# Optimization experiments

Hardware: AMD Instinct MI355X
Metric: run time of the kernel (lower is better)

The kernel has to match this reference:

```python
import jax, jax.numpy as jnp
import numpy as np

ALPHA = 0.001  # heb_lr
EPS = 1e-12    # F.normalize default eps


def setup_inputs() -> dict:
    key = jax.random.key(0)
    k1, k2 = jax.random.split(key)
    x = jax.random.normal(k1, (1, 8192), dtype=jnp.float32)
    # fc.weight ~ Uniform(0, 0.5), shape [out_dim, in_dim]
    W = jax.random.uniform(k2, (4096, 8192), dtype=jnp.float32) * 0.5
    return {"x": x, "W": W}


def reference(x, W):
    # Linear projection (no bias): [1, in] @ [in, out] -> [1, out]
    y = x @ W.T
    # F.normalize(y, p=2, dim=1)
    nrm = jnp.maximum(jnp.linalg.norm(y, axis=1, keepdims=True), EPS)
    y_n = y / nrm

    # Hebbian / Sanger (GHA) weight update, using the INITIAL weight for the
    # decorrelation term (as in the torch code).
    yv = y_n[0]  # [out]
    xv = x[0]    # [in]
    # einsum('jk,lkm,m->jl', W^T, itensors, y) with itensors[l,k,m]=1 iff k==m<=l
    # is exactly a cumulative sum over k of W[k, :] * y[k]  -> [out, in]
    sanger = yv[:, None] * jnp.cumsum(W * yv[:, None], axis=0)
    W_new = W + ALPHA * (jnp.outer(yv, xv) - sanger)
    return y_n, W_new
```

## Files before the change

kernel.cpp:

```cpp
#include <hip/hip_runtime.h>
#include <math.h>

#define ALPHA 0.001f
#define EPS 1e-12f
#define IN_DIM 8192
#define OUT_DIM 4096
#define COL4 (IN_DIM / 4)
#define NSEG 128
#define SEG_ROWS (OUT_DIM / NSEG)

typedef float f32x4 __attribute__((ext_vector_type(4)));

__global__ __launch_bounds__(256) void k_matvec(const float* __restrict__ W,
                                                const float* __restrict__ x,
                                                float* __restrict__ y) {
    const int wave = threadIdx.x >> 6;
    const int lane = threadIdx.x & 63;
    const int row = blockIdx.x * 4 + wave;
    const float4* Wr = (const float4*)(W + (size_t)row * IN_DIM);
    const float4* xv = (const float4*)x;
    float acc = 0.0f;
#pragma unroll 8
    for (int c = 0; c < COL4 / 64; ++c) {
        float4 w = Wr[lane + c * 64];
        float4 xx = xv[lane + c * 64];
        acc += w.x * xx.x + w.y * xx.y + w.z * xx.z + w.w * xx.w;
    }
#pragma unroll
    for (int off = 32; off; off >>= 1) acc += __shfl_xor(acc, off, 64);
    if (lane == 0) y[row] = acc;
}

__global__ __launch_bounds__(256) void k_norm(const float* __restrict__ y,
                                              float* __restrict__ yn_out,
                                              float* __restrict__ yv_ws) {
    __shared__ float red[4];
    float s = 0.0f;
    for (int i = threadIdx.x; i < OUT_DIM; i += 256) {
        float v = y[i];
        s += v * v;
    }
#pragma unroll
    for (int off = 32; off; off >>= 1) s += __shfl_xor(s, off, 64);
    const int wave = threadIdx.x >> 6;
    const int lane = threadIdx.x & 63;
    if (lane == 0) red[wave] = s;
    __syncthreads();
    const float tot = red[0] + red[1] + red[2] + red[3];
    const float inv = 1.0f / fmaxf(sqrtf(tot), EPS);
    for (int i = threadIdx.x; i < OUT_DIM; i += 256) {
        float v = y[i] * inv;
        yn_out[i] = v;
        yv_ws[i] = v;
    }
}

__global__ __launch_bounds__(256) void k_pseg(const float* __restrict__ W,
                                              const float* __restrict__ yv,
                                              float* __restrict__ P) {
    const int seg = blockIdx.y;
    const int col4 = blockIdx.x * 256 + threadIdx.x;
    const float4* Wp = (const float4*)W;
    const int j0 = seg * SEG_ROWS;
    float4 acc = make_float4(0.f, 0.f, 0.f, 0.f);
#pragma unroll 4
    for (int j = 0; j < SEG_ROWS; ++j) {
        const float yj = yv[j0 + j];
        float4 w = Wp[(size_t)(j0 + j) * COL4 + col4];
        acc.x += w.x * yj;
        acc.y += w.y * yj;
        acc.z += w.z * yj;
        acc.w += w.w * yj;
    }
    ((float4*)P)[(size_t)seg * COL4 + col4] = acc;
}

__global__ __launch_bounds__(64) void k_scan(float* __restrict__ P) {
    const int col4 = blockIdx.x * 64 + threadIdx.x;
    float4* Pp = (float4*)P;
    float4 run = make_float4(0.f, 0.f, 0.f, 0.f);
#pragma unroll 8
    for (int s = 0; s < NSEG; ++s) {
        float4 v = Pp[(size_t)s * COL4 + col4];
        Pp[(size_t)s * COL4 + col4] = run;
        run.x += v.x;
        run.y += v.y;
        run.z += v.z;
        run.w += v.w;
    }
}

__global__ __launch_bounds__(512) void k_update(const float* __restrict__ W,
                                                const float* __restrict__ x,
                                                const float* __restrict__ yv,
                                                const float* __restrict__ E,
                                                float* __restrict__ Wout) {
    const int seg = blockIdx.y;
    const int col4 = blockIdx.x * 512 + threadIdx.x;
    const float4* Wp = (const float4*)W;
    f32x4* Op = (f32x4*)Wout;
    float4 run = ((const float4*)E)[(size_t)seg * COL4 + col4];
    const float4 x4 = ((const float4*)x)[col4];
    const int j0 = seg * SEG_ROWS;
#pragma unroll 4
    for (int j = 0; j < SEG_ROWS; ++j) {
        const float yj = yv[j0 + j];
        const float aj = ALPHA * yj;
        const size_t idx = (size_t)(j0 + j) * COL4 + col4;
        float4 w = Wp[idx];
        run.x += w.x * yj;
        run.y += w.y * yj;
        run.z += w.z * yj;
        run.w += w.w * yj;
        f32x4 o;
        o.x = w.x + aj * (x4.x - run.x);
        o.y = w.y + aj * (x4.y - run.y);
        o.z = w.z + aj * (x4.z - run.z);
        o.w = w.w + aj * (x4.w - run.w);
        __builtin_nontemporal_store(o, &Op[idx]);
    }
}

extern "C" void kernel_launch(void* const* d_in, const int* in_sizes, int n_in,
                              void* d_out, int out_size, void* d_ws, size_t ws_size,
                              hipStream_t stream) {
    const float* x = (const float*)d_in[0];
    const float* W = (const float*)d_in[1];
    float* out = (float*)d_out;
    float* yn_out = out;
    float* Wout = out + OUT_DIM;

    float* y = (float*)d_ws;
    float* P = y + OUT_DIM;

    k_matvec<<<dim3(OUT_DIM / 4), dim3(256), 0, stream>>>(W, x, y);
    k_norm<<<dim3(1), dim3(256), 0, stream>>>(y, yn_out, y);
    k_pseg<<<dim3(COL4 / 256, NSEG), dim3(256), 0, stream>>>(W, y, P);
    k_scan<<<dim3(32), dim3(64), 0, stream>>>(P);
    k_update<<<dim3(COL4 / 512, NSEG), dim3(512), 0, stream>>>(W, x, y, P, Wout);
}
```

Measured before the change: 284.5 us.

## Fuse matvec with segment partial sums and defer normalization into update

The matvec and the per-segment weighted column sums now run in one kernel. Each block owns 8 full rows, computes the unnormalized y for each row, and reuses the same W loads to accumulate the partial prefix sums, so W is read twice instead of three times. The normalization is folded algebraically into the update kernel: the scale factors inv and inv² are applied there, and the norm kernel is replaced by a sum-of-squares pass inside the scan kernel. The partial buffer grows to 512 segments, which makes the serial scan longer and adds per-row block barriers in the fused kernel.

```diff
diff --git a/kernel.cpp b/kernel.cpp
--- a/kernel.cpp
+++ b/kernel.cpp
@@ -6,118 +6,132 @@
 #define IN_DIM 8192
 #define OUT_DIM 4096
 #define COL4 (IN_DIM / 4)
-#define NSEG 128
-#define SEG_ROWS (OUT_DIM / NSEG)
+#define NSEG 512
+#define SEG_ROWS 8
 
 typedef float f32x4 __attribute__((ext_vector_type(4)));
 
-__global__ __launch_bounds__(256) void k_matvec(const float* __restrict__ W,
-                                                const float* __restrict__ x,
-                                                float* __restrict__ y) {
-    const int wave = threadIdx.x >> 6;
-    const int lane = threadIdx.x & 63;
-    const int row = blockIdx.x * 4 + wave;
-    const float4* Wr = (const float4*)(W + (size_t)row * IN_DIM);
-    const float4* xv = (const float4*)x;
-    float acc = 0.0f;
-#pragma unroll 8
-    for (int c = 0; c < COL4 / 64; ++c) {
-        float4 w = Wr[lane + c * 64];
-        float4 xx = xv[lane + c * 64];
-        acc += w.x * xx.x + w.y * xx.y + w.z * xx.z + w.w * xx.w;
+#define WS_Y   0
+#define WS_SSQ (OUT_DIM)
+#define WS_P   (OUT_DIM + 16)
+
+__global__ __launch_bounds__(512, 4) void kA(const float* __restrict__ W,
+                                             const float* __restrict__ x,
+                                             float* __restrict__ y,
+                                             float* __restrict__ P) {
+    const int s = blockIdx.x;
+    const int t = threadIdx.x;
+    const int wv = t >> 6, ln = t & 63;
+    __shared__ float red[2][8];
+
+    const float4* W4 = (const float4*)W;
+    const float4* X4 = (const float4*)x;
+
+    float4 xr[4];
+#pragma unroll
+    for (int c = 0; c < 4; ++c) xr[c] = X4[c * 512 + t];
+
+    float4 acc[4];
+#pragma unroll
+    for (int c = 0; c < 4; ++c) acc[c] = make_float4(0.f, 0.f, 0.f, 0.f);
+
+    const int j0 = s * SEG_ROWS;
+#pragma unroll
+    for (int j = 0; j < SEG_ROWS; ++j) {
+        float4 w[4];
+#pragma unroll
+        for (int c = 0; c < 4; ++c)
+            w[c] = W4[(size_t)(j0 + j) * COL4 + c * 512 + t];
+        float p = 0.f;
+#pragma unroll
+        for (int c = 0; c < 4; ++c)
+            p += w[c].x * xr[c].x + w[c].y * xr[c].y +
+                 w[c].z * xr[c].z + w[c].w * xr[c].w;
+#pragma unroll
+        for (int off = 32; off; off >>= 1) p += __shfl_xor(p, off, 64);
+        if (ln == 0) red[j & 1][wv] = p;
+        __syncthreads();
+        float yj = 0.f;
+#pragma unroll
+        for (int k = 0; k < 8; ++k) yj += red[j & 1][k];
+        if (t == 0) y[j0 + j] = yj;
+#pragma unroll
+        for (int c = 0; c < 4; ++c) {
+            acc[c].x += w[c].x * yj;
+            acc[c].y += w[c].y * yj;
+            acc[c].z += w[c].z * yj;
+            acc[c].w += w[c].w * yj;
+        }
     }
+    float4* P4 = (float4*)P;
 #pragma unroll
-    for (int off = 32; off; off >>= 1) acc += __shfl_xor(acc, off, 64);
-    if (lane == 0) y[row] = acc;
+    for (int c = 0; c < 4; ++c)
+        P4[(size_t)s * COL4 + c * 512 + t] = acc[c];
 }
 
-__global__ __launch_bounds__(256) void k_norm(const float* __restrict__ y,
-                                              float* __restrict__ yn_out,
-                                              float* __restrict__ yv_ws) {
-    __shared__ float red[4];
-    float s = 0.0f;
-    for (int i = threadIdx.x; i < OUT_DIM; i += 256) {
-        float v = y[i];
-        s += v * v;
+__global__ __launch_bounds__(64) void kB(float* __restrict__ P,
+                                         const float* __restrict__ y,
+                                         float* __restrict__ ssq) {
+    if (blockIdx.x == 0) {
+        float q = 0.f;
+        for (int i = threadIdx.x; i < OUT_DIM; i += 64) {
+            const float v = y[i];
+            q += v * v;
+        }
+#pragma unroll
+        for (int off = 32; off; off >>= 1) q += __shfl_xor(q, off, 64);
+        if (threadIdx.x == 0) *ssq = q;
     }
-#pragma unroll
-    for (int off = 32; off; off >>= 1) s += __shfl_xor(s, off, 64);
-    const int wave = threadIdx.x >> 6;
-    const int lane = threadIdx.x & 63;
-    if (lane == 0) red[wave] = s;
-    __syncthreads();
-    const float tot = red[0] + red[1] + red[2] + red[3];
-    const float inv = 1.0f / fmaxf(sqrtf(tot), EPS);
-    for (int i = threadIdx.x; i < OUT_DIM; i += 256) {
-        float v = y[i] * inv;
-        yn_out[i] = v;
-        yv_ws[i] = v;
+    const int c4 = blockIdx.x * 64 + threadIdx.x;
+    float4* P4 = (float4*)P;
+    float4 run = make_float4(0.f, 0.f, 0.f, 0.f);
+#pragma unroll 8
+    for (int s = 0; s < NSEG; ++s) {
+        const float4 v = P4[(size_t)s * COL4 + c4];
+        P4[(size_t)s * COL4 + c4] = run;
+        run.x += v.x; run.y += v.y; run.z += v.z; run.w += v.w;
     }
 }
 
-__global__ __launch_bounds__(256) void k_pseg(const float* __restrict__ W,
-                                              const float* __restrict__ yv,
-                                              float* __restrict__ P) {
-    const int seg = blockIdx.y;
-    const int col4 = blockIdx.x * 256 + threadIdx.x;
-    const float4* Wp = (const float4*)W;
-    const int j0 = seg * SEG_ROWS;
-    float4 acc = make_float4(0.f, 0.f, 0.f, 0.f);
-#pragma unroll 4
+__global__ __launch_bounds__(512, 4) void kC(const float* __restrict__ W,
+                                             const float* __restrict__ x,
+                                             const float* __restrict__ y,
+                                             const float* __restrict__ P,
+                                             const float* __restrict__ ssq,
+                                             float* __restrict__ yn,
+                                             float* __restrict__ Wout) {
+    const int s = blockIdx.y;
+    const int t = threadIdx.x;
+    const int c4 = blockIdx.x * 512 + t;
+    const float inv = 1.f / fmaxf(sqrtf(*ssq), EPS);
+    const float a_s = ALPHA * inv;
+    const float b_s = ALPHA * inv * inv;
+    const int j0 = s * SEG_ROWS;
+
+    if (blockIdx.x == 0 && t < SEG_ROWS) {
+        yn[j0 + t] = y[j0 + t] * inv;
+    }
+
+    const float4* W4 = (const float4*)W;
+    const float4* X4 = (const float4*)x;
+    f32x4* O4 = (f32x4*)Wout;
+    float4 run = ((const float4*)P)[(size_t)s * COL4 + c4];
+    const float4 x4 = X4[c4];
+#pragma unroll
     for (int j = 0; j < SEG_ROWS; ++j) {
-        const float yj = yv[j0 + j];
-        float4 w = Wp[(size_t)(j0 + j) * COL4 + col4];
-        acc.x += w.x * yj;
-        acc.y += w.y * yj;
-        acc.z += w.z * yj;
-        acc.w += w.w * yj;
-    }
-    ((float4*)P)[(size_t)seg * COL4 + col4] = acc;
-}
-
-__global__ __launch_bounds__(64) void k_scan(float* __restrict__ P) {
-    const int col4 = blockIdx.x * 64 + threadIdx.x;
-    float4* Pp = (float4*)P;
-    float4 run = make_float4(0.f, 0.f, 0.f, 0.f);
-#pragma unroll 8
-    for (int s = 0; s < NSEG; ++s) {
-        float4 v = Pp[(size_t)s * COL4 + col4];
-        Pp[(size_t)s * COL4 + col4] = run;
-        run.x += v.x;
-        run.y += v.y;
-        run.z += v.z;
-        run.w += v.w;
-    }
-}
-
-__global__ __launch_bounds__(512) void k_update(const float* __restrict__ W,
-                                                const float* __restrict__ x,
-                                                const float* __restrict__ yv,
-                                                const float* __restrict__ E,
-                                                float* __restrict__ Wout) {
-    const int seg = blockIdx.y;
-    const int col4 = blockIdx.x * 512 + threadIdx.x;
-    const float4* Wp = (const float4*)W;
-    f32x4* Op = (f32x4*)Wout;
-    float4 run = ((const float4*)E)[(size_t)seg * COL4 + col4];
-    const float4 x4 = ((const float4*)x)[col4];
-    const int j0 = seg * SEG_ROWS;
-#pragma unroll 4
-    for (int j = 0; j < SEG_ROWS; ++j) {
-        const float yj = yv[j0 + j];
-        const float aj = ALPHA * yj;
-        const size_t idx = (size_t)(j0 + j) * COL4 + col4;
-        float4 w = Wp[idx];
-        run.x += w.x * yj;
-        run.y += w.y * yj;
-        run.z += w.z * yj;
-        run.w += w.w * yj;
+        const float yj = y[j0 + j];
+        const float aj = a_s * yj;
+        const float bj = b_s * yj;
+        const size_t idx = (size_t)(j0 + j) * COL4 + c4;
+        const float4 w = W4[idx];
+        run.x += w.x * yj; run.y += w.y * yj;
+        run.z += w.z * yj; run.w += w.w * yj;
         f32x4 o;
-        o.x = w.x + aj * (x4.x - run.x);
-        o.y = w.y + aj * (x4.y - run.y);
-        o.z = w.z + aj * (x4.z - run.z);
-        o.w = w.w + aj * (x4.w - run.w);
-        __builtin_nontemporal_store(o, &Op[idx]);
+        o.x = w.x + aj * x4.x - bj * run.x;
+        o.y = w.y + aj * x4.y - bj * run.y;
+        o.z = w.z + aj * x4.z - bj * run.z;
+        o.w = w.w + aj * x4.w - bj * run.w;
+        __builtin_nontemporal_store(o, &O4[idx]);
     }
 }
 
@@ -127,15 +141,15 @@
     const float* x = (const float*)d_in[0];
     const float* W = (const float*)d_in[1];
     float* out = (float*)d_out;
-    float* yn_out = out;
+    float* yn = out;
     float* Wout = out + OUT_DIM;
 
-    float* y = (float*)d_ws;
-    float* P = y + OUT_DIM;
+    float* ws = (float*)d_ws;
+    float* y   = ws + WS_Y;
+    float* ssq = ws + WS_SSQ;
+    float* P   = ws + WS_P;
 
-    k_matvec<<<dim3(OUT_DIM / 4), dim3(256), 0, stream>>>(W, x, y);
-    k_norm<<<dim3(1), dim3(256), 0, stream>>>(y, yn_out, y);
-    k_pseg<<<dim3(COL4 / 256, NSEG), dim3(256), 0, stream>>>(W, y, P);
-    k_scan<<<dim3(32), dim3(64), 0, stream>>>(P);
-    k_update<<<dim3(COL4 / 512, NSEG), dim3(512), 0, stream>>>(W, x, y, P, Wout);
+    kA<<<dim3(NSEG), dim3(512), 0, stream>>>(W, x, y, P);
+    kB<<<dim3(32), dim3(64), 0, stream>>>(P, y, ssq);
+    kC<<<dim3(4, NSEG), dim3(512), 0, stream>>>(W, x, y, P, ssq, yn, Wout);
 }
```

Result: slower. 305.8 us (+7.5%).
